# Optimization experiments

Hardware: AMD Instinct MI355X
Metric: run time of the kernel (lower is better)

## Reference

```python
import jax, jax.numpy as jnp
import numpy as np

SLOT_DIM = 64
EPS_SHIFT = 1e-6


def _mlp(x, Ws, bs):
    for i in range(len(Ws) - 1):
        x = jax.nn.relu(x @ Ws[i] + bs[i])
    return x @ Ws[-1] + bs[-1]


def setup_inputs() -> dict:
    key = jax.random.key(0)
    ks = jax.random.split(key, 16)
    B, C, H, W = 2, 64, 64, 64
    Q = 65536  # 256x256 output queries
    feat = jax.random.normal(ks[0], (B, C, H, W), jnp.float32)
    coord = jax.random.uniform(ks[1], (B, Q, 2), jnp.float32, -1.0, 1.0)
    cell = jnp.full((B, Q, 2), 2.0 / 256.0, jnp.float32)
    in_dim = C * 9 + 2 + 2  # unfolded feat + rel_coord + rel_cell
    dims = [in_dim, 256, 256, 256, 256, 3]
    params = {}
    for i in range(5):
        params[f"W{i}"] = jax.random.normal(ks[2 + i], (dims[i], dims[i + 1]), jnp.float32) * (1.0 / np.sqrt(dims[i]))
        params[f"b{i}"] = jnp.zeros((dims[i + 1],), jnp.float32)
    return {"feat": feat, "coord": coord, "cell": cell, **params}


def reference(feat, coord, cell, W0, b0, W1, b1, W2, b2, W3, b3, W4, b4):
    Ws = [W0, W1, W2, W3, W4]
    bs = [b0, b1, b2, b3, b4]
    B, C, H, W = feat.shape
    slot_flat = feat[:, -SLOT_DIM:].reshape(B, SLOT_DIM, H * W)
    # F.unfold(feat, 3, padding=1): channel order c*9 + ky*3 + kx
    pad = jnp.pad(feat, ((0, 0), (0, 0), (1, 1), (1, 1)))
    feat_unf = jnp.stack(
        [pad[:, :, ky:ky + H, kx:kx + W] for ky in range(3) for kx in range(3)],
        axis=2).reshape(B, C * 9, H * W)
    rx = 1.0 / H  # 2/H/2
    ry = 1.0 / W
    preds, slots = [], []
    for vx in (-1.0, 1.0):
        for vy in (-1.0, 1.0):
            cy = jnp.clip(coord[..., 0] + vx * rx + EPS_SHIFT, -1 + 1e-6, 1 - 1e-6)
            cx = jnp.clip(coord[..., 1] + vy * ry + EPS_SHIFT, -1 + 1e-6, 1 - 1e-6)
            # nearest grid_sample, align_corners=False: pix = (c+1)*N/2 - 0.5
            iy = jnp.clip(jnp.round((cy + 1.0) * H / 2.0 - 0.5), 0, H - 1).astype(jnp.int32)
            ix = jnp.clip(jnp.round((cx + 1.0) * W / 2.0 - 0.5), 0, W - 1).astype(jnp.int32)
            idx = iy * W + ix  # [B, Q]
            q_feat = jnp.take_along_axis(feat_unf, idx[:, None, :], axis=2).transpose(0, 2, 1)  # [B,Q,C*9]
            q_slot = jnp.take_along_axis(slot_flat, idx[:, None, :], axis=2).transpose(0, 2, 1)  # [B,Q,S]
            # make_coord pixel centers at sampled indices
            qc_y = -1.0 + (2.0 * iy.astype(coord.dtype) + 1.0) / H
            qc_x = -1.0 + (2.0 * ix.astype(coord.dtype) + 1.0) / W
            rel_y = (coord[..., 0] - qc_y) * H
            rel_x = (coord[..., 1] - qc_x) * W
            rel_cell = cell * jnp.asarray([H, W], coord.dtype)
            inp = jnp.concatenate([q_feat, rel_y[..., None], rel_x[..., None], rel_cell], axis=-1)
            preds.append(_mlp(inp, Ws, bs))  # [B,Q,3]
            slots.append(q_slot)
    # self-attention ensemble weighting
    slots = jnp.stack(slots, axis=-1)  # [B,Q,S,4]
    normed = slots / jnp.linalg.norm(slots, axis=-2, keepdims=True)
    n_shift = slots.shape[-1]
    attn = jnp.einsum('bqsi,bqsj->bqij', normed, normed) / SLOT_DIM  # mean over slot dim
    mask = 1.0 - jnp.eye(n_shift, dtype=attn.dtype)
    w = jnp.mean(attn * mask[None, None], axis=-1)  # [B,Q,4]
    w = w / jnp.sum(w, axis=-1, keepdims=True)
    ret = preds[0] * w[..., 0:1]
    for i in range(1, n_shift):
        ret = ret + preds[i] * w[..., i:i + 1]
    return ret
```

## Files before the change

### kernel.cpp

```cpp
#include <hip/hip_runtime.h>
#include <hip/hip_bf16.h>
#include <hip/hip_fp16.h>

typedef _Float16 f16x8 __attribute__((ext_vector_type(8)));
typedef float f32x4 __attribute__((ext_vector_type(4)));

#define OFF_FEAT_T   0u
#define OFF_FEAT_H   (2u*1024*1024)
#define OFF_G        (3u*1024*1024)
#define OFF_WP1      (7u*1024*1024)
#define OFF_WP2      (OFF_WP1 + 131072u)
#define OFF_WP3      (OFF_WP2 + 131072u)
#define OFF_WP4      (OFF_WP3 + 131072u)
#define OFF_W0PT     (OFF_WP4 + 8192u)

__device__ __forceinline__ unsigned short f2h(float v) {
  return __builtin_bit_cast(unsigned short, (_Float16)v);
}
__device__ __forceinline__ float h2f(unsigned short u) {
  return (float)__builtin_bit_cast(_Float16, u);
}

__global__ __launch_bounds__(256) void prep_kernel(
    const float* __restrict__ feat, const float* __restrict__ W0,
    const float* __restrict__ W1, const float* __restrict__ W2,
    const float* __restrict__ W3, const float* __restrict__ W4,
    char* __restrict__ ws)
{
  int flat = blockIdx.x * 256 + threadIdx.x;
  if (flat < 524288) {
    int c = flat & 63, x = (flat >> 6) & 63, y = (flat >> 12) & 63, b = flat >> 18;
    float f = feat[(((b*64 + c) << 6) + y)*64 + x];
    ((float*)(ws + OFF_FEAT_T))[flat] = f;
    ((unsigned short*)(ws + OFF_FEAT_H))[flat] = f2h(f);
    return;
  }
  int e = flat - 524288;
  if (e >= 43520) return;
  unsigned short o[8];
  char* dst;
  if (e < 24576) {
    int layer = e >> 13, ee = e & 8191;
    const float* Wsrc = layer == 0 ? W1 : (layer == 1 ? W2 : W3);
    int lane = ee & 63, nb = (ee >> 6) & 15, kk = ee >> 10;
    int n = nb*16 + (lane & 15), kb = kk*32 + ((lane >> 4) << 3);
    #pragma unroll
    for (int j = 0; j < 8; ++j) o[j] = f2h(Wsrc[(kb + j)*256 + n]);
    dst = ws + OFF_WP1 + layer*131072 + ee*16;
  } else if (e < 25088) {
    int ee = e - 24576;
    int lane = ee & 63, kk = ee >> 6;
    int n = lane & 15, kb = kk*32 + ((lane >> 4) << 3);
    #pragma unroll
    for (int j = 0; j < 8; ++j)
      o[j] = (n < 3) ? f2h(W4[(kb + j)*3 + n]) : (unsigned short)0;
    dst = ws + OFF_WP4 + ee*16;
  } else {
    int ee = e - 25088;
    int lane = ee & 63, nb = (ee >> 6) & 15, kk = ee >> 10;
    int n = nb*16 + (lane & 15), kb = kk*32 + ((lane >> 4) << 3);
    #pragma unroll
    for (int j = 0; j < 8; ++j) {
      int kp = kb + j, tap = kp >> 6, ch = kp & 63;
      o[j] = f2h(W0[(ch*9 + tap)*256 + n]);
    }
    dst = ws + OFF_W0PT + ee*16;
  }
  uint4 v;
  v.x = (unsigned)o[0] | ((unsigned)o[1] << 16);
  v.y = (unsigned)o[2] | ((unsigned)o[3] << 16);
  v.z = (unsigned)o[4] | ((unsigned)o[5] << 16);
  v.w = (unsigned)o[6] | ((unsigned)o[7] << 16);
  *(uint4*)dst = v;
}

__global__ __launch_bounds__(512) void g_kernel(char* __restrict__ ws)
{
  __shared__ __align__(16) char As[32 * 1152];
  int t = threadIdx.x, lane = t & 63, w = t >> 6;
  int bid = blockIdx.x, b = bid >> 7, rb = bid & 127;
  int y = rb >> 1, x0 = (rb & 1) << 5;
  if (t < 256) {
    int r = t >> 3, cq = t & 7;
    const unsigned short* fh = (const unsigned short*)(ws + OFF_FEAT_H);
    #pragma unroll
    for (int tap = 0; tap < 9; ++tap) {
      int dy = tap/3 - 1, dx = tap%3 - 1;
      int sy = y + dy, sx = x0 + r + dx;
      uint4 v = {0,0,0,0};
      if (sy >= 0 && sy < 64 && sx >= 0 && sx < 64)
        v = *(const uint4*)(fh + (((((b << 6) + sy) << 6) + sx) << 6) + (cq << 3));
      *(uint4*)(As + r*1152 + ((tap*128 + cq*16) ^ ((r & 7) << 4))) = v;
    }
  }
  __syncthreads();
  const f32x4 vzero = {0.f, 0.f, 0.f, 0.f};
  f32x4 acc[2][2];
  #pragma unroll
  for (int i = 0; i < 2; ++i)
    #pragma unroll
    for (int j = 0; j < 2; ++j) acc[i][j] = vzero;
  const unsigned short* wp0 = (const unsigned short*)(ws + OFF_W0PT);
  int lr = lane & 15, lg = lane >> 4;
  #pragma unroll
  for (int kk = 0; kk < 18; ++kk) {
    f16x8 a[2], bf[2];
    #pragma unroll
    for (int mf = 0; mf < 2; ++mf)
      a[mf] = *(const f16x8*)(wp0 + (((kk*16 + w*2 + mf)*64 + lane) << 3));
    #pragma unroll
    for (int nf = 0; nf < 2; ++nf) {
      int row = nf*16 + lr;
      bf[nf] = *(const f16x8*)(As + row*1152 + ((kk*64 + (lg << 4)) ^ ((row & 7) << 4)));
    }
    #pragma unroll
    for (int mf = 0; mf < 2; ++mf)
      #pragma unroll
      for (int nf = 0; nf < 2; ++nf)
        acc[mf][nf] = __builtin_amdgcn_mfma_f32_16x16x32_f16(a[mf], bf[nf], acc[mf][nf], 0, 0, 0);
  }
  unsigned short* gp = (unsigned short*)(ws + OFF_G);
  #pragma unroll
  for (int mf = 0; mf < 2; ++mf)
    #pragma unroll
    for (int nf = 0; nf < 2; ++nf) {
      int col = (w << 5) + mf*16 + (lg << 2);
      int p = (y << 6) + x0 + nf*16 + lr;
      uint2 ov;
      ov.x = (unsigned)f2h(acc[mf][nf][0]) | ((unsigned)f2h(acc[mf][nf][1]) << 16);
      ov.y = (unsigned)f2h(acc[mf][nf][2]) | ((unsigned)f2h(acc[mf][nf][3]) << 16);
      *(uint2*)(gp + ((((b << 12) + p) << 8) + col)) = ov;
    }
}

__device__ __forceinline__ void hidden_layer(const char* src, char* dst,
                                             const unsigned short* wp,
                                             const float* bias,
                                             int lane, int w)
{
  const f32x4 vzero = {0.f, 0.f, 0.f, 0.f};
  f32x4 acc[2][4];
  #pragma unroll
  for (int i = 0; i < 2; ++i)
    #pragma unroll
    for (int j = 0; j < 4; ++j) acc[i][j] = vzero;
  int lr = lane & 15, lg = lane >> 4;
  #pragma unroll
  for (int kk = 0; kk < 8; ++kk) {
    f16x8 a[2], bb[4];
    #pragma unroll
    for (int mf = 0; mf < 2; ++mf)
      a[mf] = *(const f16x8*)(wp + (((kk*16 + w*2 + mf)*64 + lane) << 3));
    #pragma unroll
    for (int nf = 0; nf < 4; ++nf) {
      int row = (nf << 4) + lr;
      bb[nf] = *(const f16x8*)(src + row*512 + ((kk*64 + (lg << 4)) ^ ((row & 7) << 4)));
    }
    #pragma unroll
    for (int mf = 0; mf < 2; ++mf)
      #pragma unroll
      for (int nf = 0; nf < 4; ++nf)
        acc[mf][nf] = __builtin_amdgcn_mfma_f32_16x16x32_f16(a[mf], bb[nf], acc[mf][nf], 0, 0, 0);
  }
  #pragma unroll
  for (int mf = 0; mf < 2; ++mf) {
    int col0 = (w << 5) + (mf << 4) + (lg << 2);
    float4 bv = *(const float4*)(bias + col0);
    int colb = col0 << 1;
    #pragma unroll
    for (int nf = 0; nf < 4; ++nf) {
      int row = (nf << 4) + lr;
      float v0 = acc[mf][nf][0] + bv.x; v0 = v0 > 0.f ? v0 : 0.f;
      float v1 = acc[mf][nf][1] + bv.y; v1 = v1 > 0.f ? v1 : 0.f;
      float v2 = acc[mf][nf][2] + bv.z; v2 = v2 > 0.f ? v2 : 0.f;
      float v3 = acc[mf][nf][3] + bv.w; v3 = v3 > 0.f ? v3 : 0.f;
      uint2 ov;
      ov.x = (unsigned)f2h(v0) | ((unsigned)f2h(v1) << 16);
      ov.y = (unsigned)f2h(v2) | ((unsigned)f2h(v3) << 16);
      *(uint2*)(dst + row*512 + (colb ^ ((row & 7) << 4))) = ov;
    }
  }
}

__global__ __launch_bounds__(512, 4) void main_kernel(
    const float* __restrict__ coord, const float* __restrict__ cell,
    const float* __restrict__ W0, const float* __restrict__ b0,
    const float* __restrict__ b1, const float* __restrict__ b2,
    const float* __restrict__ b3, const float* __restrict__ b4,
    const char* __restrict__ ws, float* __restrict__ out)
{
  __shared__ __align__(16) char bufA[64*512];
  __shared__ __align__(16) char bufB[64*512];
  __shared__ __align__(16) float rel4[64][4];
  __shared__ int prow[64];
  __shared__ float preds[64][4];
  __shared__ float dots[16][12];

  int t = threadIdx.x, lane = t & 63, w = t >> 6;
  int bid = blockIdx.x, b = bid >> 12, qt = bid & 4095;
  int qbase = qt << 4;

  if (t < 64) {
    int r = t, ql = r >> 2, s = r & 3;
    int gq = (b << 16) + qbase + ql;
    float c0 = coord[gq*2], c1 = coord[gq*2 + 1];
    float ce0 = cell[gq*2], ce1 = cell[gq*2 + 1];
    float vx = (s & 2) ? 1.0f : -1.0f;
    float vy = (s & 1) ? 1.0f : -1.0f;
    float cy = fminf(fmaxf(c0 + vx*(1.0f/64.0f) + 1e-6f, -1.0f + 1e-6f), 1.0f - 1e-6f);
    float cx = fminf(fmaxf(c1 + vy*(1.0f/64.0f) + 1e-6f, -1.0f + 1e-6f), 1.0f - 1e-6f);
    int iy = (int)fminf(fmaxf(rintf((cy + 1.0f)*32.0f - 0.5f), 0.0f), 63.0f);
    int ix = (int)fminf(fmaxf(rintf((cx + 1.0f)*32.0f - 0.5f), 0.0f), 63.0f);
    prow[r] = (iy << 6) + ix;
    float qcy = -1.0f + (float)(2*iy + 1)*(1.0f/64.0f);
    float qcx = -1.0f + (float)(2*ix + 1)*(1.0f/64.0f);
    rel4[r][0] = (c0 - qcy)*64.0f;
    rel4[r][1] = (c1 - qcx)*64.0f;
    rel4[r][2] = ce0*64.0f;
    rel4[r][3] = ce1*64.0f;
  }
  __syncthreads();
  {
    int r = t & 63;
    int ug = __builtin_amdgcn_readfirstlane(t >> 6);
    float4 rf = *(const float4*)rel4[r];
    const unsigned short* gp = (const unsigned short*)(ws + OFF_G)
                             + (((b << 12) + prow[r]) << 8);
    int swz = (r & 7) << 4;
    #pragma unroll
    for (int u = 0; u < 4; ++u) {
      int unit = u*8 + ug;
      uint4 gv = *(const uint4*)(gp + (unit << 3));
      int cb = unit << 3;
      float c0[8], c1[8], c2[8], c3[8], c4[8];
      #pragma unroll
      for (int j = 0; j < 8; ++j) {
        c0[j] = W0[576*256 + cb + j];
        c1[j] = W0[577*256 + cb + j];
        c2[j] = W0[578*256 + cb + j];
        c3[j] = W0[579*256 + cb + j];
        c4[j] = b0[cb + j];
      }
      unsigned short us[8] = {
        (unsigned short)(gv.x & 0xffff), (unsigned short)(gv.x >> 16),
        (unsigned short)(gv.y & 0xffff), (unsigned short)(gv.y >> 16),
        (unsigned short)(gv.z & 0xffff), (unsigned short)(gv.z >> 16),
        (unsigned short)(gv.w & 0xffff), (unsigned short)(gv.w >> 16) };
      unsigned short ho[8];
      #pragma unroll
      for (int j = 0; j < 8; ++j) {
        float h = h2f(us[j]) + rf.x*c0[j] + rf.y*c1[j]
                + rf.z*c2[j] + rf.w*c3[j] + c4[j];
        h = h > 0.0f ? h : 0.0f;
        ho[j] = f2h(h);
      }
      uint4 ov;
      ov.x = (unsigned)ho[0] | ((unsigned)ho[1] << 16);
      ov.y = (unsigned)ho[2] | ((unsigned)ho[3] << 16);
      ov.z = (unsigned)ho[4] | ((unsigned)ho[5] << 16);
      ov.w = (unsigned)ho[6] | ((unsigned)ho[7] << 16);
      *(uint4*)(bufA + r*512 + ((unit << 4) ^ swz)) = ov;
    }
  }
  __syncthreads();
  hidden_layer(bufA, bufB, (const unsigned short*)(ws + OFF_WP1), b1, lane, w);
  __syncthreads();
  hidden_layer(bufB, bufA, (const unsigned short*)(ws + OFF_WP2), b2, lane, w);
  __syncthreads();
  hidden_layer(bufA, bufB, (const unsigned short*)(ws + OFF_WP3), b3, lane, w);
  __syncthreads();
  if (w < 4) {
    const unsigned short* wp4 = (const unsigned short*)(ws + OFF_WP4);
    const f32x4 vzero = {0.f, 0.f, 0.f, 0.f};
    f32x4 acc = vzero;
    int lr = lane & 15, lg = lane >> 4;
    int row = (w << 4) + lr;
    #pragma unroll
    for (int kk = 0; kk < 8; ++kk) {
      f16x8 a = *(const f16x8*)(wp4 + ((kk*64 + lane) << 3));
      f16x8 bb = *(const f16x8*)(bufB + row*512 + ((kk*64 + (lg << 4)) ^ ((row & 7) << 4)));
      acc = __builtin_amdgcn_mfma_f32_16x16x32_f16(a, bb, acc, 0, 0, 0);
    }
    if (lg == 0) {
      #pragma unroll
      for (int ch = 0; ch < 3; ++ch) preds[row][ch] = acc[ch] + b4[ch];
    }
  } else {
    int tt = t - 256;
    int r = tt >> 2, q4 = tt & 3;
    const float* sp = (const float*)(ws + OFF_FEAT_T)
                    + (((b << 12) + prow[r]) << 6) + (q4 << 4);
    float* Sld = (float*)bufA;
    #pragma unroll
    for (int i = 0; i < 4; ++i)
      *(float4*)(Sld + r*76 + (q4 << 4) + (i << 2)) = *(const float4*)(sp + (i << 2));
  }
  __syncthreads();
  if (t < 160) {
    const int ia[10] = {0,1,2,3, 0,0,0,1,1,2};
    const int ib[10] = {0,1,2,3, 1,2,3,2,3,3};
    int q = t / 10, item = t - q*10;
    const float* Sld = (const float*)bufA;
    const float* ra = Sld + (q*4 + ia[item])*76;
    const float* rb = Sld + (q*4 + ib[item])*76;
    float s = 0.0f;
    #pragma unroll
    for (int i = 0; i < 16; ++i) {
      float4 va = *(const float4*)(ra + (i << 2));
      float4 vb = *(const float4*)(rb + (i << 2));
      s += va.x*vb.x + va.y*vb.y + va.z*vb.z + va.w*vb.w;
    }
    dots[q][item] = s;
  }
  __syncthreads();
  if (t < 16) {
    int q = t;
    float inv[4];
    #pragma unroll
    for (int i = 0; i < 4; ++i) inv[i] = 1.0f / sqrtf(dots[q][i]);
    const int pa[6] = {0,0,0,1,1,2};
    const int pb[6] = {1,2,3,2,3,3};
    float wgt[4] = {0.f, 0.f, 0.f, 0.f};
    #pragma unroll
    for (int pi = 0; pi < 6; ++pi) {
      float cij = dots[q][4 + pi]*inv[pa[pi]]*inv[pb[pi]];
      wgt[pa[pi]] += cij;
      wgt[pb[pi]] += cij;
    }
    float wsum = wgt[0] + wgt[1] + wgt[2] + wgt[3];
    float invw = 1.0f / wsum;
    size_t obase = (size_t)((b << 16) + qbase + q)*3;
    #pragma unroll
    for (int cch = 0; cch < 3; ++cch) {
      float v = preds[q*4 + 0][cch]*wgt[0] + preds[q*4 + 1][cch]*wgt[1]
              + preds[q*4 + 2][cch]*wgt[2] + preds[q*4 + 3][cch]*wgt[3];
      out[obase + cch] = v*invw;
    }
  }
}

extern "C" void kernel_launch(void* const* d_in, const int* in_sizes, int n_in,
                              void* d_out, int out_size, void* d_ws, size_t ws_size,
                              hipStream_t stream) {
  const float* feat  = (const float*)d_in[0];
  const float* coord = (const float*)d_in[1];
  const float* cell  = (const float*)d_in[2];
  const float* W0 = (const float*)d_in[3];
  const float* b0 = (const float*)d_in[4];
  const float* W1 = (const float*)d_in[5];
  const float* b1 = (const float*)d_in[6];
  const float* W2 = (const float*)d_in[7];
  const float* b2 = (const float*)d_in[8];
  const float* W3 = (const float*)d_in[9];
  const float* b3 = (const float*)d_in[10];
  const float* W4 = (const float*)d_in[11];
  const float* b4 = (const float*)d_in[12];
  char* ws = (char*)d_ws;
  float* out = (float*)d_out;
  prep_kernel<<<2218, 256, 0, stream>>>(feat, W0, W1, W2, W3, W4, ws);
  g_kernel<<<256, 512, 0, stream>>>(ws);
  main_kernel<<<8192, 512, 0, stream>>>(coord, cell, W0, b0, b1, b2, b3, b4, ws, out);
}
```

Measured before the change: 357.3 us.

## Switch hidden MLP layers to 32x32x16 MFMA with new weight packing and swizzle

Hidden layers and the output layer now use 32x32x16 f16 MFMA instructions in place of 16x16x32. Each wave computes a 32-row by 64-column tile, so every LDS activation fragment feeds two MFMAs. Weights are repacked in prep for the new operand layout, and the LDS swizzle changes to an XOR on the row index mod 32. Launch bounds drop from 4 to 2 blocks per CU to leave room for the larger accumulators, which risks lower occupancy.

```diff
diff --git a/kernel.cpp b/kernel.cpp
--- a/kernel.cpp
+++ b/kernel.cpp
@@ -4,6 +4,7 @@
 
 typedef _Float16 f16x8 __attribute__((ext_vector_type(8)));
 typedef float f32x4 __attribute__((ext_vector_type(4)));
+typedef float f32x16 __attribute__((ext_vector_type(16)));
 
 #define OFF_FEAT_T   0u
 #define OFF_FEAT_H   (2u*1024*1024)
@@ -12,7 +13,7 @@
 #define OFF_WP2      (OFF_WP1 + 131072u)
 #define OFF_WP3      (OFF_WP2 + 131072u)
 #define OFF_WP4      (OFF_WP3 + 131072u)
-#define OFF_W0PT     (OFF_WP4 + 8192u)
+#define OFF_W0PT     (OFF_WP4 + 16384u)
 
 __device__ __forceinline__ unsigned short f2h(float v) {
   return __builtin_bit_cast(unsigned short, (_Float16)v);
@@ -36,27 +37,29 @@
     return;
   }
   int e = flat - 524288;
-  if (e >= 43520) return;
+  if (e >= 44032) return;
   unsigned short o[8];
   char* dst;
   if (e < 24576) {
     int layer = e >> 13, ee = e & 8191;
     const float* Wsrc = layer == 0 ? W1 : (layer == 1 ? W2 : W3);
-    int lane = ee & 63, nb = (ee >> 6) & 15, kk = ee >> 10;
-    int n = nb*16 + (lane & 15), kb = kk*32 + ((lane >> 4) << 3);
-    #pragma unroll
-    for (int j = 0; j < 8; ++j) o[j] = f2h(Wsrc[(kb + j)*256 + n]);
+    int lane = ee & 63, cb = (ee >> 6) & 7, kk = ee >> 9;
+    int m = cb*32 + (lane & 31);
+    int k = kk*16 + ((lane >> 5) << 3);
+    #pragma unroll
+    for (int j = 0; j < 8; ++j) o[j] = f2h(Wsrc[(k + j)*256 + m]);
     dst = ws + OFF_WP1 + layer*131072 + ee*16;
-  } else if (e < 25088) {
+  } else if (e < 25600) {
     int ee = e - 24576;
     int lane = ee & 63, kk = ee >> 6;
-    int n = lane & 15, kb = kk*32 + ((lane >> 4) << 3);
+    int m = lane & 31;
+    int k = kk*16 + ((lane >> 5) << 3);
     #pragma unroll
     for (int j = 0; j < 8; ++j)
-      o[j] = (n < 3) ? f2h(W4[(kb + j)*3 + n]) : (unsigned short)0;
+      o[j] = (m < 3) ? f2h(W4[(k + j)*3 + m]) : (unsigned short)0;
     dst = ws + OFF_WP4 + ee*16;
   } else {
-    int ee = e - 25088;
+    int ee = e - 25600;
     int lane = ee & 63, nb = (ee >> 6) & 15, kk = ee >> 10;
     int n = nb*16 + (lane & 15), kb = kk*32 + ((lane >> 4) << 3);
     #pragma unroll
@@ -136,53 +139,43 @@
 __device__ __forceinline__ void hidden_layer(const char* src, char* dst,
                                              const unsigned short* wp,
                                              const float* bias,
-                                             int lane, int w)
+                                             int lane, int cg, int rg)
 {
-  const f32x4 vzero = {0.f, 0.f, 0.f, 0.f};
-  f32x4 acc[2][4];
-  #pragma unroll
-  for (int i = 0; i < 2; ++i)
-    #pragma unroll
-    for (int j = 0; j < 4; ++j) acc[i][j] = vzero;
-  int lr = lane & 15, lg = lane >> 4;
-  #pragma unroll
-  for (int kk = 0; kk < 8; ++kk) {
-    f16x8 a[2], bb[4];
-    #pragma unroll
-    for (int mf = 0; mf < 2; ++mf)
-      a[mf] = *(const f16x8*)(wp + (((kk*16 + w*2 + mf)*64 + lane) << 3));
-    #pragma unroll
-    for (int nf = 0; nf < 4; ++nf) {
-      int row = (nf << 4) + lr;
-      bb[nf] = *(const f16x8*)(src + row*512 + ((kk*64 + (lg << 4)) ^ ((row & 7) << 4)));
-    }
-    #pragma unroll
-    for (int mf = 0; mf < 2; ++mf)
-      #pragma unroll
-      for (int nf = 0; nf < 4; ++nf)
-        acc[mf][nf] = __builtin_amdgcn_mfma_f32_16x16x32_f16(a[mf], bb[nf], acc[mf][nf], 0, 0, 0);
+  f32x16 acc0 = {0.f}, acc1 = {0.f};
+  #pragma unroll
+  for (int i = 0; i < 16; ++i) { acc0[i] = 0.f; acc1[i] = 0.f; }
+  int ln = lane & 31, hi = lane >> 5;
+  int row = (rg << 5) + ln;
+  const char* srow = src + row*512;
+  #pragma unroll
+  for (int kk = 0; kk < 16; ++kk) {
+    f16x8 a0 = *(const f16x8*)(wp + (((kk*8 + cg*2 + 0)*64 + lane) << 3));
+    f16x8 a1 = *(const f16x8*)(wp + (((kk*8 + cg*2 + 1)*64 + lane) << 3));
+    f16x8 bb = *(const f16x8*)(srow + ((((kk << 1) + hi) ^ ln) << 4));
+    acc0 = __builtin_amdgcn_mfma_f32_32x32x16_f16(a0, bb, acc0, 0, 0, 0);
+    acc1 = __builtin_amdgcn_mfma_f32_32x32x16_f16(a1, bb, acc1, 0, 0, 0);
   }
   #pragma unroll
   for (int mf = 0; mf < 2; ++mf) {
-    int col0 = (w << 5) + (mf << 4) + (lg << 2);
-    float4 bv = *(const float4*)(bias + col0);
-    int colb = col0 << 1;
-    #pragma unroll
-    for (int nf = 0; nf < 4; ++nf) {
-      int row = (nf << 4) + lr;
-      float v0 = acc[mf][nf][0] + bv.x; v0 = v0 > 0.f ? v0 : 0.f;
-      float v1 = acc[mf][nf][1] + bv.y; v1 = v1 > 0.f ? v1 : 0.f;
-      float v2 = acc[mf][nf][2] + bv.z; v2 = v2 > 0.f ? v2 : 0.f;
-      float v3 = acc[mf][nf][3] + bv.w; v3 = v3 > 0.f ? v3 : 0.f;
+    int colbase = (cg << 6) + (mf << 5);
+    #pragma unroll
+    for (int q = 0; q < 4; ++q) {
+      int col0 = colbase + (q << 3) + (hi << 2);
+      float4 bv = *(const float4*)(bias + col0);
+      float v0 = (mf ? acc1[q*4+0] : acc0[q*4+0]) + bv.x; v0 = v0 > 0.f ? v0 : 0.f;
+      float v1 = (mf ? acc1[q*4+1] : acc0[q*4+1]) + bv.y; v1 = v1 > 0.f ? v1 : 0.f;
+      float v2 = (mf ? acc1[q*4+2] : acc0[q*4+2]) + bv.z; v2 = v2 > 0.f ? v2 : 0.f;
+      float v3 = (mf ? acc1[q*4+3] : acc0[q*4+3]) + bv.w; v3 = v3 > 0.f ? v3 : 0.f;
       uint2 ov;
       ov.x = (unsigned)f2h(v0) | ((unsigned)f2h(v1) << 16);
       ov.y = (unsigned)f2h(v2) | ((unsigned)f2h(v3) << 16);
-      *(uint2*)(dst + row*512 + (colb ^ ((row & 7) << 4))) = ov;
-    }
-  }
-}
-
-__global__ __launch_bounds__(512, 4) void main_kernel(
+      int unit = (cg << 3) + (mf << 2) + q;
+      *(uint2*)(dst + row*512 + (((unit ^ ln) << 4) + (hi << 3))) = ov;
+    }
+  }
+}
+
+__global__ __launch_bounds__(512, 2) void main_kernel(
     const float* __restrict__ coord, const float* __restrict__ cell,
     const float* __restrict__ W0, const float* __restrict__ b0,
     const float* __restrict__ b1, const float* __restrict__ b2,
@@ -197,6 +190,7 @@
   __shared__ float dots[16][12];
 
   int t = threadIdx.x, lane = t & 63, w = t >> 6;
+  int cg = w & 3, rg = w >> 2;
   int bid = blockIdx.x, b = bid >> 12, qt = bid & 4095;
   int qbase = qt << 4;
 
@@ -226,7 +220,7 @@
     float4 rf = *(const float4*)rel4[r];
     const unsigned short* gp = (const unsigned short*)(ws + OFF_G)
                              + (((b << 12) + prow[r]) << 8);
-    int swz = (r & 7) << 4;
+    int rs = r & 31;
     #pragma unroll
     for (int u = 0; u < 4; ++u) {
       int unit = u*8 + ug;
@@ -259,33 +253,36 @@
       ov.y = (unsigned)ho[2] | ((unsigned)ho[3] << 16);
       ov.z = (unsigned)ho[4] | ((unsigned)ho[5] << 16);
       ov.w = (unsigned)ho[6] | ((unsigned)ho[7] << 16);
-      *(uint4*)(bufA + r*512 + ((unit << 4) ^ swz)) = ov;
-    }
-  }
-  __syncthreads();
-  hidden_layer(bufA, bufB, (const unsigned short*)(ws + OFF_WP1), b1, lane, w);
-  __syncthreads();
-  hidden_layer(bufB, bufA, (const unsigned short*)(ws + OFF_WP2), b2, lane, w);
-  __syncthreads();
-  hidden_layer(bufA, bufB, (const unsigned short*)(ws + OFF_WP3), b3, lane, w);
-  __syncthreads();
-  if (w < 4) {
+      *(uint4*)(bufA + r*512 + ((unit ^ rs) << 4)) = ov;
+    }
+  }
+  __syncthreads();
+  hidden_layer(bufA, bufB, (const unsigned short*)(ws + OFF_WP1), b1, lane, cg, rg);
+  __syncthreads();
+  hidden_layer(bufB, bufA, (const unsigned short*)(ws + OFF_WP2), b2, lane, cg, rg);
+  __syncthreads();
+  hidden_layer(bufA, bufB, (const unsigned short*)(ws + OFF_WP3), b3, lane, cg, rg);
+  __syncthreads();
+  if (w < 2) {
     const unsigned short* wp4 = (const unsigned short*)(ws + OFF_WP4);
-    const f32x4 vzero = {0.f, 0.f, 0.f, 0.f};
-    f32x4 acc = vzero;
-    int lr = lane & 15, lg = lane >> 4;
-    int row = (w << 4) + lr;
-    #pragma unroll
-    for (int kk = 0; kk < 8; ++kk) {
+    f32x16 acc = {0.f};
+    #pragma unroll
+    for (int i = 0; i < 16; ++i) acc[i] = 0.f;
+    int ln = lane & 31, hi = lane >> 5;
+    int row = (w << 5) + ln;
+    const char* srow = bufB + row*512;
+    #pragma unroll
+    for (int kk = 0; kk < 16; ++kk) {
       f16x8 a = *(const f16x8*)(wp4 + ((kk*64 + lane) << 3));
-      f16x8 bb = *(const f16x8*)(bufB + row*512 + ((kk*64 + (lg << 4)) ^ ((row & 7) << 4)));
-      acc = __builtin_amdgcn_mfma_f32_16x16x32_f16(a, bb, acc, 0, 0, 0);
-    }
-    if (lg == 0) {
-      #pragma unroll
-      for (int ch = 0; ch < 3; ++ch) preds[row][ch] = acc[ch] + b4[ch];
-    }
-  } else {
+      f16x8 bb = *(const f16x8*)(srow + ((((kk << 1) + hi) ^ ln) << 4));
+      acc = __builtin_amdgcn_mfma_f32_32x32x16_f16(a, bb, acc, 0, 0, 0);
+    }
+    if (hi == 0) {
+      preds[row][0] = acc[0] + b4[0];
+      preds[row][1] = acc[1] + b4[1];
+      preds[row][2] = acc[2] + b4[2];
+    }
+  } else if (w >= 4) {
     int tt = t - 256;
     int r = tt >> 2, q4 = tt & 3;
     const float* sp = (const float*)(ws + OFF_FEAT_T)
@@ -357,7 +354,7 @@
   const float* b4 = (const float*)d_in[12];
   char* ws = (char*)d_ws;
   float* out = (float*)d_out;
-  prep_kernel<<<2218, 256, 0, stream>>>(feat, W0, W1, W2, W3, W4, ws);
+  prep_kernel<<<2220, 256, 0, stream>>>(feat, W0, W1, W2, W3, W4, ws);
   g_kernel<<<256, 512, 0, stream>>>(ws);
   main_kernel<<<8192, 512, 0, stream>>>(coord, cell, W0, b0, b1, b2, b3, b4, ws, out);
 }
```

Result: slower. 411.5 us (+15.2%).
